# Optimization experiments

Measured on AMD Instinct MI355X. Metric: run time of the kernel, lower is better.

Reference implementation:

```python
import jax, jax.numpy as jnp
import numpy as np

EPS = 1.1920929e-07  # torch clamp_probs eps for float32
TEMP = 0.3           # sampler temperature T


def conv1d(x, w, b, pad):
    # x: [B, Cin, L], w: [Cout, Cin, K] -> [B, Cout, L']
    y = jax.lax.conv_general_dilated(x, w, window_strides=(1,), padding=[(pad, pad)],
                                     dimension_numbers=('NCH', 'OIH', 'NCH'))
    return y + b[None, :, None]


def setup_inputs() -> dict:
    key = jax.random.key(0)
    ks = jax.random.split(key, 20)
    B, L, V, E, F, H, K = 512, 512, 100000, 100, 100, 100, 10
    p = lambda i, shape: jax.random.normal(ks[i], shape, jnp.float32) * 0.02
    return {
        'x': jax.random.randint(ks[0], (B, L), 0, V, dtype=jnp.int32),
        'u': jax.random.uniform(ks[1], (B, K, L), dtype=jnp.float32),
        'emb': p(2, (V, E)),
        'conv1_w': p(3, (F, E, 3)), 'conv1_b': p(4, (F,)),
        'gi_w': p(5, (H, F)), 'gi_b': p(6, (H,)),
        'conv2_w': p(7, (H, F, 3)), 'conv2_b': p(8, (H,)),
        'li_w': p(9, (H, H, 3)), 'li_b': p(10, (H,)),
        'conv3_w': p(11, (F, 2 * H, 1)), 'conv3_b': p(12, (F,)),
        'conv4_w': p(13, (1, F, 1)), 'conv4_b': p(14, (1,)),
        'fc1_w': p(15, (H, E)), 'fc1_b': p(16, (H,)),
        'head_w': p(17, (1, H)), 'head_b': p(18, (1,)),
    }


def _ti_logits(e, conv1_w, conv1_b, gi_w, gi_b, conv2_w, conv2_b,
               li_w, li_b, conv3_w, conv3_b, conv4_w, conv4_b):
    relu = jax.nn.relu
    xt = jnp.swapaxes(e, 1, 2)                       # [B, E, L]
    h = relu(conv1d(xt, conv1_w, conv1_b, 1))        # [B, F, L]
    g = relu(h.mean(axis=-1) @ gi_w.T + gi_b)        # [B, H] (AdaptiveAvgPool1d(1))
    loc = relu(conv1d(relu(conv1d(h, conv2_w, conv2_b, 1)), li_w, li_b, 1))  # [B, H, L]
    gexp = jnp.broadcast_to(g[:, :, None], loc.shape)
    z = jnp.concatenate([gexp, loc], axis=1)         # [B, 2H, L]
    z = relu(conv1d(z, conv3_w, conv3_b, 0))
    return conv1d(z, conv4_w, conv4_b, 0)            # [B, 1, L]


def reference(x, u, emb, conv1_w, conv1_b, gi_w, gi_b, conv2_w, conv2_b,
              li_w, li_b, conv3_w, conv3_b, conv4_w, conv4_b,
              fc1_w, fc1_b, head_w, head_b):
    e = emb[x]                                       # [B, L, E] embedding gather
    logits = _ti_logits(e, conv1_w, conv1_b, gi_w, gi_b, conv2_w, conv2_b,
                        li_w, li_b, conv3_w, conv3_b, conv4_w, conv4_b)
    # Gumbel top-k continuous sampling (training path)
    uc = jnp.clip(u, EPS, 1.0 - EPS)
    gumbel = -jnp.log(-jnp.log(uc))                  # [B, K, L]
    noisy = (gumbel + logits) / TEMP                 # logits [B,1,L] broadcasts over K
    csamples = jax.nn.softmax(noisy, axis=-1).max(axis=1)  # [B, L]
    # distil predictor: masked mean pooling + MLP + sigmoid head
    pooled = (e * csamples[:, :, None]).mean(axis=1)  # [B, E]
    h = jax.nn.relu(pooled @ fc1_w.T + fc1_b)
    out = jax.nn.sigmoid(h @ head_w.T + head_b)       # [B, 1]
    return out, csamples
```

## Files before the change

### kernel.cpp

```cpp
#include <hip/hip_runtime.h>
#include <math.h>

#define DEV __device__ __forceinline__

typedef __attribute__((ext_vector_type(8))) short short8;
typedef __attribute__((ext_vector_type(4))) short short4v;
typedef __attribute__((ext_vector_type(4))) float f32x4;
typedef __attribute__((ext_vector_type(2))) unsigned uint2v;

#define SSTR 136

DEV short f2bf(float f) {
    unsigned u = __builtin_bit_cast(unsigned, f);
    unsigned r = (u + 0x7fffu + ((u >> 16) & 1u)) >> 16;
    return (short)r;
}

#if __has_builtin(__builtin_amdgcn_cvt_pk_bf16_f32)
DEV unsigned pk2bf(float a, float b) {
    auto v = __builtin_amdgcn_cvt_pk_bf16_f32(a, b);
    return __builtin_bit_cast(unsigned, v);
}
#else
DEV unsigned pk2bf(float a, float b) {
    return ((unsigned)(unsigned short)f2bf(a)) |
           (((unsigned)(unsigned short)f2bf(b)) << 16);
}
#endif

DEV float bfu(short s) {
    unsigned u = ((unsigned)(unsigned short)s) << 16;
    return __builtin_bit_cast(float, u);
}

__global__ __launch_bounds__(256) void emb_cvt_kernel(
    const float* __restrict__ emb, short* __restrict__ embT) {
    int t = threadIdx.x;
    int row = blockIdx.x * 8 + (t >> 5);
    int c4 = t & 31;
    if (c4 >= 28) return;
    short4v v = {0, 0, 0, 0};
    if (c4 < 25) {
        f32x4 e = *(const f32x4*)&emb[row * 100 + c4 * 4];
#pragma unroll
        for (int r = 0; r < 4; ++r) v[r] = f2bf(e[r]);
    }
    *(short4v*)&embT[row * 112 + c4 * 4] = v;
}

__global__ __launch_bounds__(64) void pack_all_kernel(
    const float* __restrict__ c1w, const float* __restrict__ c2w,
    const float* __restrict__ liw, const float* __restrict__ c3w,
    short* __restrict__ A1, short* __restrict__ A2,
    short* __restrict__ A3, short* __restrict__ A4) {
    int bx = blockIdx.x;
    const float* w; short* dst; int mode, lbx;
    if (bx < 70)       { w = c1w; dst = A1; mode = 0; lbx = bx; }
    else if (bx < 140) { w = c2w; dst = A2; mode = 0; lbx = bx - 70; }
    else if (bx < 210) { w = liw; dst = A3; mode = 0; lbx = bx - 140; }
    else               { w = c3w; dst = A4; mode = 1; lbx = bx - 210; }
    int lane = threadIdx.x;
    int f = lbx % 7 * 16 + (lane & 15);
    int kb = (lbx / 7) * 32 + (lane >> 4) * 8;
    short8 v;
#pragma unroll
    for (int j = 0; j < 8; ++j) {
        int kk = kb + j;
        float val = 0.f;
        if (f < 100) {
            if (mode == 0) {
                int oct = kk >> 3, dk = oct / 13;
                int c = (oct - 13 * dk) * 8 + (kk & 7);
                if (dk < 3 && c < 100) val = w[(f * 100 + c) * 3 + dk];
            } else {
                if (kk < 100) val = w[f * 200 + 100 + kk];
            }
        }
        v[j] = f2bf(val);
    }
    *(short8*)&dst[(lbx * 64 + lane) * 8] = v;
}

template<int NT, bool POOL, bool TO_GLOBAL, bool EDGE>
DEV void conv3tap(const short* __restrict__ Ap, const short* s_src,
                  short* s_dst, short* __restrict__ gout,
                  const int* bofs, const int* bofs4,
                  const f32x4 bs0, const f32x4 bs1,
                  int row0l, int l0, float* __restrict__ hpart, int pbase,
                  int lane, int wv) {
    const int q = lane >> 4, n = lane & 15;
    const int mt0 = wv * 2;
    const bool two = (wv < 3);
    const f32x4 z4 = {0.f, 0.f, 0.f, 0.f};
    f32x4 acc0[NT], acc1[NT];
#pragma unroll
    for (int nt = 0; nt < NT; ++nt) { acc0[nt] = bs0; acc1[nt] = bs1; }
#pragma unroll
    for (int ks = 0; ks < 10; ++ks) {
        short8 a0 = *(const short8*)&Ap[(ks * 448 + mt0 * 64 + lane) * 8];
        short8 a1;
        if (two) a1 = *(const short8*)&Ap[(ks * 448 + (mt0 + 1) * 64 + lane) * 8];
        const char* bp = (const char*)s_src + bofs[ks];
#pragma unroll
        for (int nt = 0; nt < NT; ++nt) {
            short8 bf;
            if (nt < 4) bf = *(const short8*)(bp + nt * (16 * SSTR * 2));
            else        bf = *(const short8*)((const char*)s_src + bofs4[ks]);
            acc0[nt] = __builtin_amdgcn_mfma_f32_16x16x32_bf16(a0, bf, acc0[nt], 0, 0, 0);
            if (two)
                acc1[nt] = __builtin_amdgcn_mfma_f32_16x16x32_bf16(a1, bf, acc1[nt], 0, 0, 0);
        }
    }
    const int fb0 = mt0 * 16 + q * 4, fb1 = fb0 + 16;
    f32x4 ps0 = z4, ps1 = z4;
#pragma unroll
    for (int nt = 0; nt < NT; ++nt) {
        const int j = nt * 16 + n;
        f32x4 v0, v1;
#pragma unroll
        for (int r = 0; r < 4; ++r) {
            v0[r] = fmaxf(acc0[nt][r], 0.f);
            if (two) v1[r] = fmaxf(acc1[nt][r], 0.f);
        }
        if constexpr (EDGE) {
            const bool lok = (unsigned)(row0l + j) < 512u;
#pragma unroll
            for (int r = 0; r < 4; ++r) {
                v0[r] = lok ? v0[r] : 0.f;
                if (two) v1[r] = lok ? v1[r] : 0.f;
            }
        }
        if constexpr (POOL) {
            const int l = row0l + j;
            const bool pok = (l >= l0) && (l < l0 + 64);
            if (pok) {
#pragma unroll
                for (int r = 0; r < 4; ++r) {
                    ps0[r] += v0[r];
                    if (two) ps1[r] += v1[r];
                }
            }
        }
        uint2v pk0, pk1;
        pk0[0] = pk2bf(v0[0], v0[1]); pk0[1] = pk2bf(v0[2], v0[3]);
        if (two) { pk1[0] = pk2bf(v1[0], v1[1]); pk1[1] = pk2bf(v1[2], v1[3]); }
        if constexpr (TO_GLOBAL) {
            *(uint2v*)&gout[j * 112 + fb0] = pk0;
            if (two) *(uint2v*)&gout[j * 112 + fb1] = pk1;
        } else {
            if (nt < 4 || n < 6) {
                *(uint2v*)&s_dst[j * SSTR + fb0] = pk0;
                if (two) *(uint2v*)&s_dst[j * SSTR + fb1] = pk1;
            }
        }
    }
    if constexpr (POOL) {
#pragma unroll
        for (int off = 1; off <= 8; off <<= 1)
#pragma unroll
            for (int r = 0; r < 4; ++r) {
                ps0[r] += __shfl_xor(ps0[r], off, 64);
                ps1[r] += __shfl_xor(ps1[r], off, 64);
            }
        if (n == 0) {
            *(f32x4*)&hpart[pbase * 112 + fb0] = ps0;
            if (two) *(f32x4*)&hpart[pbase * 112 + fb1] = ps1;
        }
    }
}

__global__ __launch_bounds__(256, 4) void fused_conv_kernel(
    const int* __restrict__ xidx, const short* __restrict__ embT,
    const short* __restrict__ A1, const short* __restrict__ A2,
    const short* __restrict__ A3,
    const float* __restrict__ b1, const float* __restrict__ b2,
    const float* __restrict__ b3,
    short* __restrict__ locT, float* __restrict__ hpart) {
    extern __shared__ char smem[];
    short* s_e = (short*)smem;
    short* s_h = (short*)(smem + 72 * SSTR * 2);
    const int tid = threadIdx.x;
    const int b = blockIdx.y, bx = blockIdx.x, l0 = bx * 64;
    const int lane = tid & 63, wv = tid >> 6;
    const int q = lane >> 4, n = lane & 15;

#pragma unroll
    for (int p = 0; p < 5; ++p) {
        int idx = tid + p * 256;
        int j = idx >> 4, c8 = idx & 15;
        if (j < 70 && c8 < 14) {
            int lg = l0 - 3 + j;
            short8 v = {0, 0, 0, 0, 0, 0, 0, 0};
            if (lg >= 0 && lg < 512) {
                int row = xidx[b * 512 + lg];
                v = *(const short8*)&embT[row * 112 + c8 * 8];
            }
            *(short8*)&s_e[j * SSTR + c8 * 8] = v;
        }
    }

    int bofs[10], bofs4[10];
#pragma unroll
    for (int ks = 0; ks < 10; ++ks) {
        int oct = ks * 4 + q;
        int dk = (oct >= 39) ? 3 : (oct >= 26) ? 2 : (oct >= 13) ? 1 : 0;
        int c0 = (oct - 13 * dk) * 8;
        bofs[ks] = ((n + dk) * SSTR + c0) * 2;
        int r4 = 64 + n + dk; if (r4 > 69) r4 = 69;
        bofs4[ks] = (r4 * SSTR + c0) * 2;
    }
    const int fb0 = wv * 32 + q * 4, fb1 = fb0 + 16;
    const f32x4 z4 = {0.f, 0.f, 0.f, 0.f};
    f32x4 bsA0 = (fb0 < 100) ? *(const f32x4*)&b1[fb0] : z4;
    f32x4 bsA1 = (fb1 < 100) ? *(const f32x4*)&b1[fb1] : z4;
    f32x4 bsB0 = (fb0 < 100) ? *(const f32x4*)&b2[fb0] : z4;
    f32x4 bsB1 = (fb1 < 100) ? *(const f32x4*)&b2[fb1] : z4;
    f32x4 bsC0 = (fb0 < 100) ? *(const f32x4*)&b3[fb0] : z4;
    f32x4 bsC1 = (fb1 < 100) ? *(const f32x4*)&b3[fb1] : z4;

    __syncthreads();
    const bool edge = (bx == 0) || (bx == 7);
    if (edge) {
        conv3tap<5, true, false, true>(A1, s_e, s_h, nullptr, bofs, bofs4,
                                       bsA0, bsA1, l0 - 2, l0, hpart,
                                       b * 8 + bx, lane, wv);
        __syncthreads();
        conv3tap<5, false, false, true>(A2, s_h, s_e, nullptr, bofs, bofs4,
                                        bsB0, bsB1, l0 - 1, l0, nullptr, 0,
                                        lane, wv);
    } else {
        conv3tap<5, true, false, false>(A1, s_e, s_h, nullptr, bofs, bofs4,
                                        bsA0, bsA1, l0 - 2, l0, hpart,
                                        b * 8 + bx, lane, wv);
        __syncthreads();
        conv3tap<5, false, false, false>(A2, s_h, s_e, nullptr, bofs, bofs4,
                                         bsB0, bsB1, l0 - 1, l0, nullptr, 0,
                                         lane, wv);
    }
    __syncthreads();
    conv3tap<4, false, true, false>(A3, s_e, nullptr,
                                    locT + ((size_t)b * 512 + l0) * 112,
                                    bofs, bofs4, bsC0, bsC1, l0, l0,
                                    nullptr, 0, lane, wv);
}

__global__ __launch_bounds__(256, 4) void conv3_logits_kernel(
    const short* __restrict__ locT, const short* __restrict__ A4,
    const float* __restrict__ zg, const float* __restrict__ w4,
    const float* __restrict__ b4, float* __restrict__ logits) {
    extern __shared__ char smem[];
    short* s_in = (short*)smem;
    float* s_part = (float*)(smem + 128 * SSTR * 2);
    const int tid = threadIdx.x;
    const int b = blockIdx.y, l0r = blockIdx.x * 128;
    const int lane = tid & 63, wv = tid >> 6;
    const int q = lane >> 4, n = lane & 15;

    {
        short8 tmp[8];
#pragma unroll
        for (int p = 0; p < 8; ++p) {
            int idx = tid + p * 256;
            int j = idx >> 4, c8 = idx & 15;
            if (c8 < 14)
                tmp[p] = *(const short8*)&locT[((size_t)b * 512 + l0r + j) * 112 + c8 * 8];
        }
#pragma unroll
        for (int p = 0; p < 8; ++p) {
            int idx = tid + p * 256;
            int j = idx >> 4, c8 = idx & 15;
            if (c8 < 14)
                *(short8*)&s_in[j * SSTR + c8 * 8] = tmp[p];
        }
    }
    const f32x4 z4 = {0.f, 0.f, 0.f, 0.f};
    const int mt0 = wv * 2;
    const bool two = (wv < 3);
    const int fb0 = mt0 * 16 + q * 4, fb1 = fb0 + 16;
    f32x4 zg0 = *(const f32x4*)&zg[b * 112 + fb0];
    f32x4 zg1 = two ? *(const f32x4*)&zg[b * 112 + fb1] : z4;
    f32x4 acc0[8], acc1[8];
#pragma unroll
    for (int nt = 0; nt < 8; ++nt) { acc0[nt] = zg0; acc1[nt] = zg1; }
    __syncthreads();

#pragma unroll
    for (int ks = 0; ks < 4; ++ks) {
        short8 a0 = *(const short8*)&A4[(ks * 448 + mt0 * 64 + lane) * 8];
        short8 a1;
        if (two) a1 = *(const short8*)&A4[(ks * 448 + (mt0 + 1) * 64 + lane) * 8];
        int c0 = (ks * 4 + q) * 8;
        if (c0 > 104) c0 = 104;
        const short* bptr = s_in + n * SSTR + c0;
#pragma unroll
        for (int nt = 0; nt < 8; ++nt) {
            short8 bf = *(const short8*)(bptr + nt * 16 * SSTR);
            acc0[nt] = __builtin_amdgcn_mfma_f32_16x16x32_bf16(a0, bf, acc0[nt], 0, 0, 0);
            if (two)
                acc1[nt] = __builtin_amdgcn_mfma_f32_16x16x32_bf16(a1, bf, acc1[nt], 0, 0, 0);
        }
    }
    f32x4 w40 = (fb0 < 100) ? *(const f32x4*)&w4[fb0] : z4;
    f32x4 w41 = (two && fb1 < 100) ? *(const f32x4*)&w4[fb1] : z4;
#pragma unroll
    for (int nt = 0; nt < 8; ++nt) {
        float part = 0.f;
#pragma unroll
        for (int r = 0; r < 4; ++r) {
            part += fmaxf(acc0[nt][r], 0.f) * w40[r];
            if (two) part += fmaxf(acc1[nt][r], 0.f) * w41[r];
        }
        part += __shfl_xor(part, 16, 64);
        part += __shfl_xor(part, 32, 64);
        if (q == 0) s_part[wv * 128 + nt * 16 + n] = part;
    }
    __syncthreads();
    if (tid < 128) {
        float s = s_part[tid] + s_part[128 + tid] + s_part[256 + tid] +
                  s_part[384 + tid] + b4[0];
        logits[b * 512 + l0r + tid] = s;
    }
}

__global__ __launch_bounds__(128) void pool_gate_kernel(
    const float* __restrict__ hpart, const float* __restrict__ gi_w,
    const float* __restrict__ gi_b, const float* __restrict__ w3,
    const float* __restrict__ b3, float* __restrict__ zg) {
    int b = blockIdx.x, tid = threadIdx.x;
    __shared__ float s_hm[112];
    __shared__ float s_g[100];
    if (tid < 112) {
        float a = 0.f;
#pragma unroll
        for (int s = 0; s < 8; ++s) a += hpart[(b * 8 + s) * 112 + tid];
        s_hm[tid] = a * (1.f / 512.f);
    }
    __syncthreads();
    if (tid < 100) {
        float a = gi_b[tid];
        for (int f = 0; f < 100; ++f) a += s_hm[f] * gi_w[tid * 100 + f];
        s_g[tid] = fmaxf(a, 0.f);
    }
    __syncthreads();
    if (tid < 112) {
        float a = 0.f;
        if (tid < 100) {
            a = b3[tid];
            for (int h = 0; h < 100; ++h) a += s_g[h] * w3[tid * 200 + h];
        }
        zg[b * 112 + tid] = a;
    }
}

__global__ __launch_bounds__(256) void samp_head_kernel(
    const float* __restrict__ u, const float* __restrict__ logits,
    const int* __restrict__ xidx, const short* __restrict__ embT,
    const float* __restrict__ f1w, const float* __restrict__ f1b,
    const float* __restrict__ hw, const float* __restrict__ hb,
    float* __restrict__ cs_out, float* __restrict__ out) {
    const float EPSV = 1.1920929e-07f;
    int b = blockIdx.x, tid = threadIdx.x;
    int lane = tid & 63, wv = tid >> 6;
    __shared__ float s_log[512], s_cs[512], s_red[8];
    __shared__ int s_x[512];
    __shared__ float s_acc[16][112];
    __shared__ float s_pool[112], s_h2[100], s_fin[4];
    float uu[20];
#pragma unroll
    for (int k = 0; k < 10; ++k) {
        uu[k * 2]     = u[(b * 10 + k) * 512 + tid];
        uu[k * 2 + 1] = u[(b * 10 + k) * 512 + tid + 256];
    }
    for (int l = tid; l < 512; l += 256) {
        s_log[l] = logits[b * 512 + l];
        s_cs[l] = 0.f;
        s_x[l] = xidx[b * 512 + l];
    }
    __syncthreads();
    for (int k = 0; k < 10; ++k) {
        float nz[2];
#pragma unroll
        for (int i = 0; i < 2; ++i) {
            int l = tid + i * 256;
            float vv = fminf(fmaxf(uu[k * 2 + i], EPSV), 1.f - EPSV);
            float g = -__logf(-__logf(vv));
            nz[i] = (g + s_log[l]) * (1.f / 0.3f);
        }
        float m = fmaxf(nz[0], nz[1]);
#pragma unroll
        for (int off = 32; off >= 1; off >>= 1) m = fmaxf(m, __shfl_xor(m, off, 64));
        if (lane == 0) s_red[wv] = m;
        __syncthreads();
        m = fmaxf(fmaxf(s_red[0], s_red[1]), fmaxf(s_red[2], s_red[3]));
        float e0 = __expf(nz[0] - m), e1 = __expf(nz[1] - m);
        float s = e0 + e1;
#pragma unroll
        for (int off = 32; off >= 1; off >>= 1) s += __shfl_xor(s, off, 64);
        if (lane == 0) s_red[4 + wv] = s;
        __syncthreads();
        float inv = 1.f / (s_red[4] + s_red[5] + s_red[6] + s_red[7]);
        s_cs[tid]       = fmaxf(s_cs[tid],       e0 * inv);
        s_cs[tid + 256] = fmaxf(s_cs[tid + 256], e1 * inv);
    }
    for (int l = tid; l < 512; l += 256) cs_out[b * 512 + l] = s_cs[l];
    __syncthreads();
    int jg = tid >> 4, c8 = tid & 15;
    if (c8 < 14) {
        f32x4 pa = {0.f, 0.f, 0.f, 0.f}, pb = {0.f, 0.f, 0.f, 0.f};
#pragma unroll 4
        for (int l = jg; l < 512; l += 16) {
            int row = s_x[l];
            float cv = s_cs[l];
            short8 e8 = *(const short8*)&embT[(size_t)row * 112 + c8 * 8];
#pragma unroll
            for (int r = 0; r < 4; ++r) {
                pa[r] += cv * bfu(e8[r]);
                pb[r] += cv * bfu(e8[4 + r]);
            }
        }
        *(f32x4*)&s_acc[jg][c8 * 8] = pa;
        *(f32x4*)&s_acc[jg][c8 * 8 + 4] = pb;
    }
    __syncthreads();
    if (tid < 112) {
        float p = 0.f;
#pragma unroll
        for (int g = 0; g < 16; ++g) p += s_acc[g][tid];
        s_pool[tid] = p * (1.f / 512.f);
    }
    __syncthreads();
    if (tid < 100) {
        float a = f1b[tid];
        for (int i = 0; i < 100; ++i) a += s_pool[i] * f1w[tid * 100 + i];
        s_h2[tid] = fmaxf(a, 0.f);
    }
    __syncthreads();
    float v = (tid < 100) ? s_h2[tid] * hw[tid] : 0.f;
#pragma unroll
    for (int off = 32; off >= 1; off >>= 1) v += __shfl_xor(v, off, 64);
    if (lane == 0) s_fin[wv] = v;
    __syncthreads();
    if (tid == 0) {
        float z = s_fin[0] + s_fin[1] + s_fin[2] + s_fin[3] + hb[0];
        out[b] = 1.f / (1.f + __expf(-z));
    }
}

extern "C" void kernel_launch(void* const* d_in, const int* in_sizes, int n_in,
                              void* d_out, int out_size, void* d_ws, size_t ws_size,
                              hipStream_t stream) {
    const int*   x   = (const int*)d_in[0];
    const float* u   = (const float*)d_in[1];
    const float* emb = (const float*)d_in[2];
    const float* c1w = (const float*)d_in[3];
    const float* c1b = (const float*)d_in[4];
    const float* giw = (const float*)d_in[5];
    const float* gib = (const float*)d_in[6];
    const float* c2w = (const float*)d_in[7];
    const float* c2b = (const float*)d_in[8];
    const float* liw = (const float*)d_in[9];
    const float* lib = (const float*)d_in[10];
    const float* c3w = (const float*)d_in[11];
    const float* c3b = (const float*)d_in[12];
    const float* c4w = (const float*)d_in[13];
    const float* c4b = (const float*)d_in[14];
    const float* f1w = (const float*)d_in[15];
    const float* f1b = (const float*)d_in[16];
    const float* hww = (const float*)d_in[17];
    const float* hbb = (const float*)d_in[18];
    float* out = (float*)d_out;

    char* ws = (char*)d_ws;
    short* locT   = (short*)(ws + 0);
    short* embT   = (short*)(ws + 58720256);
    short* A1     = (short*)(ws + 81120256);
    short* A2     = (short*)(ws + 81191936);
    short* A3     = (short*)(ws + 81263616);
    short* A4     = (short*)(ws + 81335296);
    float* zg     = (float*)(ws + 81363968);
    float* logits = (float*)(ws + 81593344);
    float* hpart  = (float*)(ws + 82641920);

    emb_cvt_kernel<<<12500, 256, 0, stream>>>(emb, embT);
    pack_all_kernel<<<238, 64, 0, stream>>>(c1w, c2w, liw, c3w, A1, A2, A3, A4);

    size_t smemA = 2 * 72 * SSTR * 2;
    fused_conv_kernel<<<dim3(8, 512), 256, smemA, stream>>>(
        x, embT, A1, A2, A3, c1b, c2b, lib, locT, hpart);
    pool_gate_kernel<<<512, 128, 0, stream>>>(hpart, giw, gib, c3w, c3b, zg);
    size_t smemB = 128 * SSTR * 2 + 4 * 128 * 4;
    conv3_logits_kernel<<<dim3(4, 512), 256, smemB, stream>>>(
        locT, A4, zg, c4w, c4b, logits);
    samp_head_kernel<<<512, 256, 0, stream>>>(
        u, logits, x, embT, f1w, f1b, hww, hbb, out + 512, out);
}
```

Measured before the change: 277.2 us.

## Rebalance MFMA wave tiling in conv kernels and per-wave softmax in sampler

```diff
diff --git a/kernel.cpp b/kernel.cpp
--- a/kernel.cpp
+++ b/kernel.cpp
@@ -9,6 +9,7 @@
 typedef __attribute__((ext_vector_type(2))) unsigned uint2v;
 
 #define SSTR 136
+#define ROWB (16 * SSTR * 2)
 
 DEV short f2bf(float f) {
     unsigned u = __builtin_bit_cast(unsigned, f);
@@ -81,90 +82,93 @@
     *(short8*)&dst[(lbx * 64 + lane) * 8] = v;
 }
 
-template<int NT, bool POOL, bool TO_GLOBAL, bool EDGE>
-DEV void conv3tap(const short* __restrict__ Ap, const short* s_src,
-                  short* s_dst, short* __restrict__ gout,
-                  const int* bofs, const int* bofs4,
-                  const f32x4 bs0, const f32x4 bs1,
-                  int row0l, int l0, float* __restrict__ hpart, int pbase,
-                  int lane, int wv) {
+template<int MT, int NT, int MTB, int NTB, bool CLAMPL, bool POOL,
+         bool TO_GLOBAL, bool EDGE>
+DEV void ctap(const short* __restrict__ Ap, const short* s_src, short* s_dst,
+              short* __restrict__ gout, const int* bofs, const int* bofs4,
+              const float* __restrict__ bias, int row0l, int l0,
+              float* __restrict__ hpart_slot, int lane) {
     const int q = lane >> 4, n = lane & 15;
-    const int mt0 = wv * 2;
-    const bool two = (wv < 3);
     const f32x4 z4 = {0.f, 0.f, 0.f, 0.f};
-    f32x4 acc0[NT], acc1[NT];
-#pragma unroll
-    for (int nt = 0; nt < NT; ++nt) { acc0[nt] = bs0; acc1[nt] = bs1; }
+    f32x4 acc[MT][NT];
+#pragma unroll
+    for (int mt = 0; mt < MT; ++mt) {
+        int fb = (MTB + mt) * 16 + q * 4;
+        f32x4 bs = (fb < 100) ? *(const f32x4*)&bias[fb] : z4;
+#pragma unroll
+        for (int nt = 0; nt < NT; ++nt) acc[mt][nt] = bs;
+    }
 #pragma unroll
     for (int ks = 0; ks < 10; ++ks) {
-        short8 a0 = *(const short8*)&Ap[(ks * 448 + mt0 * 64 + lane) * 8];
-        short8 a1;
-        if (two) a1 = *(const short8*)&Ap[(ks * 448 + (mt0 + 1) * 64 + lane) * 8];
+        short8 a[MT];
+#pragma unroll
+        for (int mt = 0; mt < MT; ++mt)
+            a[mt] = *(const short8*)&Ap[(ks * 448 + (MTB + mt) * 64 + lane) * 8];
         const char* bp = (const char*)s_src + bofs[ks];
+        short8 bf[NT];
 #pragma unroll
         for (int nt = 0; nt < NT; ++nt) {
-            short8 bf;
-            if (nt < 4) bf = *(const short8*)(bp + nt * (16 * SSTR * 2));
-            else        bf = *(const short8*)((const char*)s_src + bofs4[ks]);
-            acc0[nt] = __builtin_amdgcn_mfma_f32_16x16x32_bf16(a0, bf, acc0[nt], 0, 0, 0);
-            if (two)
-                acc1[nt] = __builtin_amdgcn_mfma_f32_16x16x32_bf16(a1, bf, acc1[nt], 0, 0, 0);
-        }
-    }
-    const int fb0 = mt0 * 16 + q * 4, fb1 = fb0 + 16;
-    f32x4 ps0 = z4, ps1 = z4;
+            if (CLAMPL && (NTB + nt) == 4)
+                bf[nt] = *(const short8*)((const char*)s_src + bofs4[ks]);
+            else
+                bf[nt] = *(const short8*)(bp + (NTB + nt) * ROWB);
+        }
+#pragma unroll
+        for (int mt = 0; mt < MT; ++mt)
+#pragma unroll
+            for (int nt = 0; nt < NT; ++nt)
+                acc[mt][nt] = __builtin_amdgcn_mfma_f32_16x16x32_bf16(
+                    a[mt], bf[nt], acc[mt][nt], 0, 0, 0);
+    }
+    f32x4 ps[MT];
+    if constexpr (POOL) {
+#pragma unroll
+        for (int mt = 0; mt < MT; ++mt) ps[mt] = z4;
+    }
 #pragma unroll
     for (int nt = 0; nt < NT; ++nt) {
-        const int j = nt * 16 + n;
-        f32x4 v0, v1;
-#pragma unroll
-        for (int r = 0; r < 4; ++r) {
-            v0[r] = fmaxf(acc0[nt][r], 0.f);
-            if (two) v1[r] = fmaxf(acc1[nt][r], 0.f);
-        }
-        if constexpr (EDGE) {
-            const bool lok = (unsigned)(row0l + j) < 512u;
+        const int j = (NTB + nt) * 16 + n;
+        const int l = row0l + j;
+        bool lok = true;
+        if constexpr (EDGE) lok = ((unsigned)l < 512u);
+        const bool pok = POOL && (l >= l0) && (l < l0 + 64);
+#pragma unroll
+        for (int mt = 0; mt < MT; ++mt) {
+            const int fb = (MTB + mt) * 16 + q * 4;
+            f32x4 v;
 #pragma unroll
             for (int r = 0; r < 4; ++r) {
-                v0[r] = lok ? v0[r] : 0.f;
-                if (two) v1[r] = lok ? v1[r] : 0.f;
+                v[r] = fmaxf(acc[mt][nt][r], 0.f);
+                if constexpr (EDGE) v[r] = lok ? v[r] : 0.f;
             }
-        }
-        if constexpr (POOL) {
-            const int l = row0l + j;
-            const bool pok = (l >= l0) && (l < l0 + 64);
-            if (pok) {
-#pragma unroll
-                for (int r = 0; r < 4; ++r) {
-                    ps0[r] += v0[r];
-                    if (two) ps1[r] += v1[r];
+            if constexpr (POOL) {
+                if (pok) {
+#pragma unroll
+                    for (int r = 0; r < 4; ++r) ps[mt][r] += v[r];
                 }
             }
-        }
-        uint2v pk0, pk1;
-        pk0[0] = pk2bf(v0[0], v0[1]); pk0[1] = pk2bf(v0[2], v0[3]);
-        if (two) { pk1[0] = pk2bf(v1[0], v1[1]); pk1[1] = pk2bf(v1[2], v1[3]); }
-        if constexpr (TO_GLOBAL) {
-            *(uint2v*)&gout[j * 112 + fb0] = pk0;
-            if (two) *(uint2v*)&gout[j * 112 + fb1] = pk1;
-        } else {
-            if (nt < 4 || n < 6) {
-                *(uint2v*)&s_dst[j * SSTR + fb0] = pk0;
-                if (two) *(uint2v*)&s_dst[j * SSTR + fb1] = pk1;
+            uint2v pk;
+            pk[0] = pk2bf(v[0], v[1]); pk[1] = pk2bf(v[2], v[3]);
+            if constexpr (TO_GLOBAL) {
+                *(uint2v*)&gout[j * 112 + fb] = pk;
+            } else {
+                if ((NTB + nt) < 4 || n < 6)
+                    *(uint2v*)&s_dst[j * SSTR + fb] = pk;
             }
         }
     }
     if constexpr (POOL) {
 #pragma unroll
-        for (int off = 1; off <= 8; off <<= 1)
-#pragma unroll
-            for (int r = 0; r < 4; ++r) {
-                ps0[r] += __shfl_xor(ps0[r], off, 64);
-                ps1[r] += __shfl_xor(ps1[r], off, 64);
-            }
+        for (int mt = 0; mt < MT; ++mt)
+#pragma unroll
+            for (int off = 1; off <= 8; off <<= 1)
+#pragma unroll
+                for (int r = 0; r < 4; ++r)
+                    ps[mt][r] += __shfl_xor(ps[mt][r], off, 64);
         if (n == 0) {
-            *(f32x4*)&hpart[pbase * 112 + fb0] = ps0;
-            if (two) *(f32x4*)&hpart[pbase * 112 + fb1] = ps1;
+#pragma unroll
+            for (int mt = 0; mt < MT; ++mt)
+                *(f32x4*)&hpart_slot[(MTB + mt) * 16 + q * 4] = ps[mt];
         }
     }
 }
@@ -209,39 +213,84 @@
         int r4 = 64 + n + dk; if (r4 > 69) r4 = 69;
         bofs4[ks] = (r4 * SSTR + c0) * 2;
     }
-    const int fb0 = wv * 32 + q * 4, fb1 = fb0 + 16;
+    float* hps = hpart + ((b * 8 + bx) * 2 + (wv & 1)) * 112;
+    short* gouts = locT + ((size_t)b * 512 + l0) * 112;
+
+    __syncthreads();
+    const bool edge = (bx == 0) || (bx == 7);
+
+#define PASS3T(Ap, SRC, DST, BIAS, R0L, PL, E)                                   \
+    if (wv == 0)      ctap<4,3,0,0,false,PL,false,E>(Ap,SRC,DST,nullptr,bofs,bofs4,BIAS,R0L,l0,hps,lane); \
+    else if (wv == 1) ctap<4,2,0,3,true, PL,false,E>(Ap,SRC,DST,nullptr,bofs,bofs4,BIAS,R0L,l0,hps,lane); \
+    else if (wv == 2) ctap<3,3,4,0,false,PL,false,E>(Ap,SRC,DST,nullptr,bofs,bofs4,BIAS,R0L,l0,hps,lane); \
+    else              ctap<3,2,4,3,true, PL,false,E>(Ap,SRC,DST,nullptr,bofs,bofs4,BIAS,R0L,l0,hps,lane);
+
+    if (edge) {
+        PASS3T(A1, s_e, s_h, b1, l0 - 2, true, true)
+        __syncthreads();
+        PASS3T(A2, s_h, s_e, b2, l0 - 1, false, true)
+    } else {
+        PASS3T(A1, s_e, s_h, b1, l0 - 2, true, false)
+        __syncthreads();
+        PASS3T(A2, s_h, s_e, b2, l0 - 1, false, false)
+    }
+    __syncthreads();
+    if (wv == 0)      ctap<4,2,0,0,false,false,true,false>(A3,s_e,nullptr,gouts,bofs,bofs4,b3,l0,l0,hps,lane);
+    else if (wv == 1) ctap<4,2,0,2,false,false,true,false>(A3,s_e,nullptr,gouts,bofs,bofs4,b3,l0,l0,hps,lane);
+    else if (wv == 2) ctap<3,2,4,0,false,false,true,false>(A3,s_e,nullptr,gouts,bofs,bofs4,b3,l0,l0,hps,lane);
+    else              ctap<3,2,4,2,false,false,true,false>(A3,s_e,nullptr,gouts,bofs,bofs4,b3,l0,l0,hps,lane);
+#undef PASS3T
+}
+
+template<int MT, int MTB, int NTB, int SLOT>
+DEV void c3tile(const short* s_in, float* s_part, const short* __restrict__ A4,
+                const float* __restrict__ zg, const float* __restrict__ w4,
+                int bb, int lane) {
+    const int q = lane >> 4, n = lane & 15;
     const f32x4 z4 = {0.f, 0.f, 0.f, 0.f};
-    f32x4 bsA0 = (fb0 < 100) ? *(const f32x4*)&b1[fb0] : z4;
-    f32x4 bsA1 = (fb1 < 100) ? *(const f32x4*)&b1[fb1] : z4;
-    f32x4 bsB0 = (fb0 < 100) ? *(const f32x4*)&b2[fb0] : z4;
-    f32x4 bsB1 = (fb1 < 100) ? *(const f32x4*)&b2[fb1] : z4;
-    f32x4 bsC0 = (fb0 < 100) ? *(const f32x4*)&b3[fb0] : z4;
-    f32x4 bsC1 = (fb1 < 100) ? *(const f32x4*)&b3[fb1] : z4;
-
-    __syncthreads();
-    const bool edge = (bx == 0) || (bx == 7);
-    if (edge) {
-        conv3tap<5, true, false, true>(A1, s_e, s_h, nullptr, bofs, bofs4,
-                                       bsA0, bsA1, l0 - 2, l0, hpart,
-                                       b * 8 + bx, lane, wv);
-        __syncthreads();
-        conv3tap<5, false, false, true>(A2, s_h, s_e, nullptr, bofs, bofs4,
-                                        bsB0, bsB1, l0 - 1, l0, nullptr, 0,
-                                        lane, wv);
-    } else {
-        conv3tap<5, true, false, false>(A1, s_e, s_h, nullptr, bofs, bofs4,
-                                        bsA0, bsA1, l0 - 2, l0, hpart,
-                                        b * 8 + bx, lane, wv);
-        __syncthreads();
-        conv3tap<5, false, false, false>(A2, s_h, s_e, nullptr, bofs, bofs4,
-                                         bsB0, bsB1, l0 - 1, l0, nullptr, 0,
-                                         lane, wv);
-    }
-    __syncthreads();
-    conv3tap<4, false, true, false>(A3, s_e, nullptr,
-                                    locT + ((size_t)b * 512 + l0) * 112,
-                                    bofs, bofs4, bsC0, bsC1, l0, l0,
-                                    nullptr, 0, lane, wv);
+    f32x4 acc[MT][4];
+#pragma unroll
+    for (int mt = 0; mt < MT; ++mt) {
+        int fb = (MTB + mt) * 16 + q * 4;
+        f32x4 zgv = *(const f32x4*)&zg[bb * 112 + fb];
+#pragma unroll
+        for (int nt = 0; nt < 4; ++nt) acc[mt][nt] = zgv;
+    }
+#pragma unroll
+    for (int ks = 0; ks < 4; ++ks) {
+        short8 a[MT];
+#pragma unroll
+        for (int mt = 0; mt < MT; ++mt)
+            a[mt] = *(const short8*)&A4[(ks * 448 + (MTB + mt) * 64 + lane) * 8];
+        int c0 = (ks * 4 + q) * 8;
+        if (c0 > 104) c0 = 104;
+        const char* bp = (const char*)(s_in + n * SSTR + c0);
+        short8 bf[4];
+#pragma unroll
+        for (int nt = 0; nt < 4; ++nt)
+            bf[nt] = *(const short8*)(bp + (NTB + nt) * ROWB);
+#pragma unroll
+        for (int mt = 0; mt < MT; ++mt)
+#pragma unroll
+            for (int nt = 0; nt < 4; ++nt)
+                acc[mt][nt] = __builtin_amdgcn_mfma_f32_16x16x32_bf16(
+                    a[mt], bf[nt], acc[mt][nt], 0, 0, 0);
+    }
+#pragma unroll
+    for (int nt = 0; nt < 4; ++nt) {
+        float part = 0.f;
+#pragma unroll
+        for (int mt = 0; mt < MT; ++mt) {
+            const int fb = (MTB + mt) * 16 + q * 4;
+            f32x4 w4v = (fb < 100) ? *(const f32x4*)&w4[fb] : z4;
+#pragma unroll
+            for (int r = 0; r < 4; ++r)
+                part += fmaxf(acc[mt][nt][r], 0.f) * w4v[r];
+        }
+        part += __shfl_xor(part, 16, 64);
+        part += __shfl_xor(part, 32, 64);
+        if (q == 0) s_part[SLOT * 128 + (NTB + nt) * 16 + n] = part;
+    }
 }
 
 __global__ __launch_bounds__(256, 4) void conv3_logits_kernel(
@@ -254,7 +303,6 @@
     const int tid = threadIdx.x;
     const int b = blockIdx.y, l0r = blockIdx.x * 128;
     const int lane = tid & 63, wv = tid >> 6;
-    const int q = lane >> 4, n = lane & 15;
 
     {
         short8 tmp[8];
@@ -273,53 +321,14 @@
                 *(short8*)&s_in[j * SSTR + c8 * 8] = tmp[p];
         }
     }
-    const f32x4 z4 = {0.f, 0.f, 0.f, 0.f};
-    const int mt0 = wv * 2;
-    const bool two = (wv < 3);
-    const int fb0 = mt0 * 16 + q * 4, fb1 = fb0 + 16;
-    f32x4 zg0 = *(const f32x4*)&zg[b * 112 + fb0];
-    f32x4 zg1 = two ? *(const f32x4*)&zg[b * 112 + fb1] : z4;
-    f32x4 acc0[8], acc1[8];
-#pragma unroll
-    for (int nt = 0; nt < 8; ++nt) { acc0[nt] = zg0; acc1[nt] = zg1; }
-    __syncthreads();
-
-#pragma unroll
-    for (int ks = 0; ks < 4; ++ks) {
-        short8 a0 = *(const short8*)&A4[(ks * 448 + mt0 * 64 + lane) * 8];
-        short8 a1;
-        if (two) a1 = *(const short8*)&A4[(ks * 448 + (mt0 + 1) * 64 + lane) * 8];
-        int c0 = (ks * 4 + q) * 8;
-        if (c0 > 104) c0 = 104;
-        const short* bptr = s_in + n * SSTR + c0;
-#pragma unroll
-        for (int nt = 0; nt < 8; ++nt) {
-            short8 bf = *(const short8*)(bptr + nt * 16 * SSTR);
-            acc0[nt] = __builtin_amdgcn_mfma_f32_16x16x32_bf16(a0, bf, acc0[nt], 0, 0, 0);
-            if (two)
-                acc1[nt] = __builtin_amdgcn_mfma_f32_16x16x32_bf16(a1, bf, acc1[nt], 0, 0, 0);
-        }
-    }
-    f32x4 w40 = (fb0 < 100) ? *(const f32x4*)&w4[fb0] : z4;
-    f32x4 w41 = (two && fb1 < 100) ? *(const f32x4*)&w4[fb1] : z4;
-#pragma unroll
-    for (int nt = 0; nt < 8; ++nt) {
-        float part = 0.f;
-#pragma unroll
-        for (int r = 0; r < 4; ++r) {
-            part += fmaxf(acc0[nt][r], 0.f) * w40[r];
-            if (two) part += fmaxf(acc1[nt][r], 0.f) * w41[r];
-        }
-        part += __shfl_xor(part, 16, 64);
-        part += __shfl_xor(part, 32, 64);
-        if (q == 0) s_part[wv * 128 + nt * 16 + n] = part;
-    }
-    __syncthreads();
-    if (tid < 128) {
-        float s = s_part[tid] + s_part[128 + tid] + s_part[256 + tid] +
-                  s_part[384 + tid] + b4[0];
-        logits[b * 512 + l0r + tid] = s;
-    }
+    __syncthreads();
+    if (wv == 0)      c3tile<4, 0, 0, 0>(s_in, s_part, A4, zg, w4, b, lane);
+    else if (wv == 1) c3tile<4, 0, 4, 0>(s_in, s_part, A4, zg, w4, b, lane);
+    else if (wv == 2) c3tile<3, 4, 0, 1>(s_in, s_part, A4, zg, w4, b, lane);
+    else              c3tile<3, 4, 4, 1>(s_in, s_part, A4, zg, w4, b, lane);
+    __syncthreads();
+    if (tid < 128)
+        logits[b * 512 + l0r + tid] = s_part[tid] + s_part[128 + tid] + b4[0];
 }
 
 __global__ __launch_bounds__(128) void pool_gate_kernel(
@@ -332,7 +341,7 @@
     if (tid < 112) {
         float a = 0.f;
 #pragma unroll
-        for (int s = 0; s < 8; ++s) a += hpart[(b * 8 + s) * 112 + tid];
+        for (int s = 0; s < 16; ++s) a += hpart[(b * 16 + s) * 112 + tid];
         s_hm[tid] = a * (1.f / 512.f);
     }
     __syncthreads();
@@ -359,50 +368,60 @@
     const float* __restrict__ hw, const float* __restrict__ hb,
     float* __restrict__ cs_out, float* __restrict__ out) {
     const float EPSV = 1.1920929e-07f;
+    const float INVT = 1.f / 0.3f;
     int b = blockIdx.x, tid = threadIdx.x;
     int lane = tid & 63, wv = tid >> 6;
-    __shared__ float s_log[512], s_cs[512], s_red[8];
+    __shared__ float s_logT[512], s_cs[512];
     __shared__ int s_x[512];
+    __shared__ float s_csw[4][512];
     __shared__ float s_acc[16][112];
     __shared__ float s_pool[112], s_h2[100], s_fin[4];
-    float uu[20];
-#pragma unroll
-    for (int k = 0; k < 10; ++k) {
-        uu[k * 2]     = u[(b * 10 + k) * 512 + tid];
-        uu[k * 2 + 1] = u[(b * 10 + k) * 512 + tid + 256];
-    }
     for (int l = tid; l < 512; l += 256) {
-        s_log[l] = logits[b * 512 + l];
-        s_cs[l] = 0.f;
+        s_logT[l] = logits[b * 512 + l] * INVT;
         s_x[l] = xidx[b * 512 + l];
     }
     __syncthreads();
-    for (int k = 0; k < 10; ++k) {
-        float nz[2];
-#pragma unroll
-        for (int i = 0; i < 2; ++i) {
-            int l = tid + i * 256;
-            float vv = fminf(fmaxf(uu[k * 2 + i], EPSV), 1.f - EPSV);
-            float g = -__logf(-__logf(vv));
-            nz[i] = (g + s_log[l]) * (1.f / 0.3f);
-        }
-        float m = fmaxf(nz[0], nz[1]);
-#pragma unroll
-        for (int off = 32; off >= 1; off >>= 1) m = fmaxf(m, __shfl_xor(m, off, 64));
-        if (lane == 0) s_red[wv] = m;
-        __syncthreads();
-        m = fmaxf(fmaxf(s_red[0], s_red[1]), fmaxf(s_red[2], s_red[3]));
-        float e0 = __expf(nz[0] - m), e1 = __expf(nz[1] - m);
-        float s = e0 + e1;
-#pragma unroll
-        for (int off = 32; off >= 1; off >>= 1) s += __shfl_xor(s, off, 64);
-        if (lane == 0) s_red[4 + wv] = s;
-        __syncthreads();
-        float inv = 1.f / (s_red[4] + s_red[5] + s_red[6] + s_red[7]);
-        s_cs[tid]       = fmaxf(s_cs[tid],       e0 * inv);
-        s_cs[tid + 256] = fmaxf(s_cs[tid + 256], e1 * inv);
-    }
-    for (int l = tid; l < 512; l += 256) cs_out[b * 512 + l] = s_cs[l];
+    const int nk = (wv < 2) ? 3 : 2;
+    float csl[8];
+#pragma unroll
+    for (int i = 0; i < 8; ++i) csl[i] = 0.f;
+    float lt[8];
+#pragma unroll
+    for (int i = 0; i < 8; ++i) lt[i] = s_logT[lane * 8 + i];
+    for (int j = 0; j < nk; ++j) {
+        int k = wv + 4 * j;
+        f32x4 u0 = *(const f32x4*)&u[(b * 10 + k) * 512 + lane * 8];
+        f32x4 u1 = *(const f32x4*)&u[(b * 10 + k) * 512 + lane * 8 + 4];
+        float nz[8];
+#pragma unroll
+        for (int i = 0; i < 8; ++i) {
+            float vv = (i < 4) ? u0[i] : u1[i - 4];
+            vv = fminf(fmaxf(vv, EPSV), 1.f - EPSV);
+            nz[i] = -__logf(-__logf(vv)) * INVT + lt[i];
+        }
+        float m = nz[0];
+#pragma unroll
+        for (int i = 1; i < 8; ++i) m = fmaxf(m, nz[i]);
+#pragma unroll
+        for (int off = 1; off <= 32; off <<= 1) m = fmaxf(m, __shfl_xor(m, off, 64));
+        float e[8], s = 0.f;
+#pragma unroll
+        for (int i = 0; i < 8; ++i) { e[i] = __expf(nz[i] - m); s += e[i]; }
+#pragma unroll
+        for (int off = 1; off <= 32; off <<= 1) s += __shfl_xor(s, off, 64);
+        float inv = 1.f / s;
+#pragma unroll
+        for (int i = 0; i < 8; ++i) csl[i] = fmaxf(csl[i], e[i] * inv);
+    }
+#pragma unroll
+    for (int i = 0; i < 8; ++i) s_csw[wv][lane * 8 + i] = csl[i];
+    __syncthreads();
+    for (int l = tid; l < 512; l += 256) {
+        float c = fmaxf(fmaxf(s_csw[0][l], s_csw[1][l]),
+                        fmaxf(s_csw[2][l], s_csw[3][l]));
+        s_cs[l] = c;
+        cs_out[b * 512 + l] = c;
+    }
     __syncthreads();
     int jg = tid >> 4, c8 = tid & 15;
     if (c8 < 14) {
@@ -488,7 +507,7 @@
     fused_conv_kernel<<<dim3(8, 512), 256, smemA, stream>>>(
         x, embT, A1, A2, A3, c1b, c2b, lib, locT, hpart);
     pool_gate_kernel<<<512, 128, 0, stream>>>(hpart, giw, gib, c3w, c3b, zg);
-    size_t smemB = 128 * SSTR * 2 + 4 * 128 * 4;
+    size_t smemB = 128 * SSTR * 2 + 2 * 128 * 4;
     conv3_logits_kernel<<<dim3(4, 512), 256, smemB, stream>>>(
         locT, A4, zg, c4w, c4b, logits);
     samp_head_kernel<<<512, 256, 0, stream>>>(
```

After: 253.8 us. 1.09x faster.
